# Kernel optimization log

Hardware: AMD Instinct MI355X
Metric: run time of the kernel (lower is better)

Reference implementation:

```python
import jax, jax.numpy as jnp
import numpy as np

TAU = 2.0   # LIF membrane time constant
VTH = 1.0   # spike threshold
EPS = 1e-5
T = 2       # spiking timesteps
H = 8       # attention heads
L = 4       # transformer depth
SCALE = 0.125
GW = 0.8    # graph branch weight


def _spike(v):
    # heaviside forward, sigmoid surrogate backward (spikingjelly-style)
    sg = jax.nn.sigmoid(4.0 * (v - VTH))
    return sg + jax.lax.stop_gradient((v >= VTH).astype(v.dtype) - sg)


def lif(x):
    # multi-step LIF over leading time axis, hard reset, detach_reset=True
    def step(v, xt):
        v = v + (xt - v) / TAU
        s = _spike(v)
        v = v * (1.0 - jax.lax.stop_gradient(s))
        return v, s
    _, s = jax.lax.scan(step, jnp.zeros_like(x[0]), x)
    return s


def bn(x, g, b):
    # batch-norm (training stats) over all dims but the channel dim
    ax = tuple(range(x.ndim - 1))
    m = x.mean(ax, keepdims=True)
    v = x.var(ax, keepdims=True)
    return (x - m) * jax.lax.rsqrt(v + EPS) * g + b


def ln(x, g, b):
    m = x.mean(-1, keepdims=True)
    v = x.var(-1, keepdims=True)
    return (x - m) * jax.lax.rsqrt(v + EPS) * g + b


def gcn_agg(x, row, col, n):
    # symmetric-normalized sparse aggregation: out[col] += x[row] / sqrt(d[row]d[col])
    deg = jax.ops.segment_sum(jnp.ones_like(col, dtype=x.dtype), col, num_segments=n)
    dinv = jnp.where(deg > 0, jax.lax.rsqrt(deg), 0.0)
    val = dinv[col] * dinv[row]
    return jax.ops.segment_sum(val[:, None] * x[row], col, num_segments=n)


def _forward(fl, edge_index):
    (x, fc0_w, fc0_b, ln_g, ln_b, wq, wk, wv, wo,
     bnq_g, bnq_b, bnk_g, bnk_b, bnv_g, bnv_b, bno_g, bno_b,
     w1, bn1_g, bn1_b, w2, bn2_g, bn2_b, head_w, head_b,
     gfc_w, gfc_b, gbn0_g, gbn0_b, gconv_w, gconv_b, gbn_g, gbn_b,
     fc_w, fc_b) = fl
    N = x.shape[0]
    row, col = edge_index[0], edge_index[1]
    # ---- spiking transformer branch: x -> [T,N,D] ----
    h = jnp.broadcast_to(x, (T,) + x.shape) @ fc0_w + fc0_b
    h = jax.nn.relu(ln(h, ln_g, ln_b))
    D = h.shape[-1]
    for l in range(L):
        s = lif(h)
        q = lif(bn(s @ wq[l], bnq_g[l], bnq_b[l])).reshape(T, N, H, D // H)
        k = lif(bn(s @ wk[l], bnk_g[l], bnk_b[l])).reshape(T, N, H, D // H)
        v = lif(bn(s @ wv[l], bnv_g[l], bnv_b[l])).reshape(T, N, H, D // H)
        # linear (token-sum) spiking self-attention: kv = K^T V per head/timestep
        kv = jnp.einsum('tnhd,tnhe->thde', k, v)
        o = (jnp.einsum('tnhd,thde->tnhe', q, kv) * SCALE).reshape(T, N, D)
        o = bn(lif(o) @ wo[l], bno_g[l], bno_b[l])
        h = h + o
        m = bn(lif(h) @ w1[l], bn1_g[l], bn1_b[l])
        m = bn(lif(m) @ w2[l], bn2_g[l], bn2_b[l])
        h = h + m
    x1 = (lif(h) @ head_w + head_b).mean(0)   # [N, C], mean over T (TET=False)
    # ---- sparse GNN diffusion branch ----
    g0 = jax.nn.relu(bn(x @ gfc_w + gfc_b, gbn0_g, gbn0_b))
    g = g0
    for i in range(2):
        g = gcn_agg(g, row, col, N) @ gconv_w[i] + gconv_b[i]
        g = jax.nn.relu(bn(g, gbn_g[i], gbn_b[i]))
        g = g + g0  # residual to first layer
    out = GW * g + (1.0 - GW) * x1
    return out @ fc_w + fc_b


def setup_inputs() -> dict:
    key = jax.random.key(0)
    ks = iter(jax.random.split(key, 64))
    N, F, D, C = 16384, 512, 512, 40
    DH = 2 * D
    r = lambda *s: jax.random.normal(next(ks), s, dtype=jnp.float32)
    inp = {
        'x': r(N, F),
        'fc0_w': r(F, D) * 0.02, 'fc0_b': jnp.zeros((D,), jnp.float32),
        'ln_g': jnp.ones((D,), jnp.float32), 'ln_b': jnp.zeros((D,), jnp.float32),
        'wq': r(L, D, D) * 0.02, 'wk': r(L, D, D) * 0.02,
        'wv': r(L, D, D) * 0.02, 'wo': r(L, D, D) * 0.02,
        'bnq_g': 1.0 + 0.1 * r(L, D), 'bnq_b': 0.02 * r(L, D),
        'bnk_g': 1.0 + 0.1 * r(L, D), 'bnk_b': 0.02 * r(L, D),
        'bnv_g': 1.0 + 0.1 * r(L, D), 'bnv_b': 0.02 * r(L, D),
        'bno_g': 1.0 + 0.1 * r(L, D), 'bno_b': 0.02 * r(L, D),
        'w1': r(L, D, DH) * 0.02, 'bn1_g': 1.0 + 0.1 * r(L, DH), 'bn1_b': 0.02 * r(L, DH),
        'w2': r(L, DH, D) * 0.02, 'bn2_g': 1.0 + 0.1 * r(L, D), 'bn2_b': 0.02 * r(L, D),
        'head_w': r(D, C) * 0.02, 'head_b': jnp.zeros((C,), jnp.float32),
        'gfc_w': r(F, C) * 0.02, 'gfc_b': jnp.zeros((C,), jnp.float32),
        'gbn0_g': jnp.ones((C,), jnp.float32), 'gbn0_b': jnp.zeros((C,), jnp.float32),
        'gconv_w': r(2, C, C) * 0.1, 'gconv_b': jnp.zeros((2, C), jnp.float32),
        'gbn_g': 1.0 + 0.1 * r(2, C), 'gbn_b': 0.02 * r(2, C),
        'fc_w': r(C, C) * 0.1, 'fc_b': jnp.zeros((C,), jnp.float32),
        'edge_index': jax.random.randint(next(ks), (2, 262144), 0, N, dtype=jnp.int32),
    }
    return inp


def reference(x, fc0_w, fc0_b, ln_g, ln_b, wq, wk, wv, wo, bnq_g, bnq_b, bnk_g, bnk_b, bnv_g, bnv_b, bno_g, bno_b, w1, bn1_g, bn1_b, w2, bn2_g, bn2_b, head_w, head_b, gfc_w, gfc_b, gbn0_g, gbn0_b, gconv_w, gconv_b, gbn_g, gbn_b, fc_w, fc_b, edge_index):
    fl = (x, fc0_w, fc0_b, ln_g, ln_b, wq, wk, wv, wo, bnq_g, bnq_b, bnk_g, bnk_b, bnv_g, bnv_b, bno_g, bno_b, w1, bn1_g, bn1_b, w2, bn2_g, bn2_b, head_w, head_b, gfc_w, gfc_b, gbn0_g, gbn0_b, gconv_w, gconv_b, gbn_g, gbn_b, fc_w, fc_b)
    return _forward(fl, edge_index)
```

## Files before the change

kernel.cpp:

```cpp
#include <hip/hip_runtime.h>
#include <cstddef>
#include <cstdint>

constexpr int N_NODES = 16384;
constexpr int D_MODEL = 512;
constexpr int C_OUT   = 40;
constexpr int CW      = 256;
constexpr int ND      = N_NODES * D_MODEL;
constexpr int M2      = 2 * N_NODES;

typedef int i32x4 __attribute__((ext_vector_type(4)));

#define S0 0.001953125
#define S1 1.52587890625e-05
#define S2 1.1920928955078125e-07
#define S3 9.31322574615478515625e-10
#define S4 7.2759576141834259033203125e-12

#define WD_Q 0
#define WD_K 1310720
#define WD_V 2621440
#define WD_O 3932160
#define WD_1 5242880
#define WD_2 7864320
#define WD_TOTAL 10485760

__global__ __launch_bounds__(256)
void w_digits_layer(const float* __restrict__ wq, const float* __restrict__ wk,
                    const float* __restrict__ wv, const float* __restrict__ wo,
                    const float* __restrict__ w1, const float* __restrict__ w2,
                    uint8_t* __restrict__ Wd) {
    int idx = blockIdx.x * 256 + threadIdx.x;
    const float* W;
    uint8_t* outb;
    int N, rem;
    if (idx < 1048576) {
        int mm = idx >> 18;
        rem = idx & 262143;
        const float* ptrs[4] = {wq, wk, wv, wo};
        W = ptrs[mm]; outb = Wd + (size_t)mm * 1310720; N = 512;
    } else if (idx < 1572864) {
        rem = idx - 1048576; W = w1; outb = Wd + WD_1; N = 1024;
    } else if (idx < 2097152) {
        rem = idx - 1572864; W = w2; outb = Wd + WD_2; N = 512;
    } else return;
    int k = rem / N, n = rem - k * N;
    double r = (double)W[rem];
    uint8_t* out = outb + (((size_t)(k >> 4) * N + n) * 5) * 16 + (k & 15);
    const double scl[5] = {512.0, 65536.0, 8388608.0, 1073741824.0, 137438953472.0};
    const double inv[5] = {S0, S1, S2, S3, S4};
#pragma unroll
    for (int j = 0; j < 5; ++j) {
        int d = (int)rint(r * scl[j]);
        d = d > 127 ? 127 : (d < -127 ? -127 : d);
        r -= (double)d * inv[j];
        out[j * 16] = (uint8_t)(int8_t)d;
    }
}

__global__ __launch_bounds__(256)
void gemm_i8_bits(const uint64_t* __restrict__ bits, int kWords,
                  const uint8_t* __restrict__ Wd, int Nmat, int colOff,
                  double* __restrict__ C, int ldc, int K,
                  double* __restrict__ sum, double* __restrict__ sumsq) {
    const int lane = threadIdx.x & 63;
    const int wv   = threadIdx.x >> 6;
    const int m    = lane & 15;
    const int q    = lane >> 4;
    const int row  = blockIdx.y * 64 + wv * 16 + m;
    const int colB = blockIdx.x * 64;

    i32x4 acc[4][5];
#pragma unroll
    for (int t = 0; t < 4; ++t)
#pragma unroll
        for (int j = 0; j < 5; ++j) acc[t][j] = (i32x4){0, 0, 0, 0};

    const uint64_t* brow = bits + (size_t)row * kWords;
    const size_t colBase = (size_t)(colOff + colB + m);

    for (int kb = 0; kb < K; kb += 64) {
        uint64_t wbits = brow[kb >> 6];
        uint32_t hw = (uint32_t)(wbits >> (q * 16)) & 0xFFFFu;
        i32x4 afrag;
#pragma unroll
        for (int i = 0; i < 4; ++i)
            afrag[i] = (int)((((hw >> (4 * i)) & 0xFu) * 0x00204081u) & 0x01010101u);

        const size_t kb4 = (size_t)(kb >> 4) + q;
        const uint8_t* bp = Wd + (kb4 * Nmat + colBase) * 80;
#pragma unroll
        for (int t = 0; t < 4; ++t) {
            const uint8_t* bt = bp + (size_t)t * 16 * 80;
#pragma unroll
            for (int j = 0; j < 5; ++j) {
                i32x4 bfrag = *reinterpret_cast<const i32x4*>(bt + j * 16);
                acc[t][j] = __builtin_amdgcn_mfma_i32_16x16x64_i8(afrag, bfrag, acc[t][j], 0, 0, 0);
            }
        }
    }

    const int orow = blockIdx.y * 64 + wv * 16 + q * 4;
    double sarr[4], qarr[4];
#pragma unroll
    for (int t = 0; t < 4; ++t) {
        double s = 0.0, qs = 0.0;
        double* Cc = C + (size_t)orow * ldc + colB + t * 16 + m;
#pragma unroll
        for (int i = 0; i < 4; ++i) {
            double p = (double)acc[t][0][i] * S0 + (double)acc[t][1][i] * S1
                     + (double)acc[t][2][i] * S2 + (double)acc[t][3][i] * S3
                     + (double)acc[t][4][i] * S4;
            Cc[(size_t)i * ldc] = p;
            s += p; qs += p * p;
        }
        sarr[t] = s; qarr[t] = qs;
    }
    __shared__ double ls[4][64], lq[4][64];
#pragma unroll
    for (int t = 0; t < 4; ++t) {
        double s = sarr[t], qq = qarr[t];
        s  += __shfl_xor(s, 16);  s  += __shfl_xor(s, 32);
        qq += __shfl_xor(qq, 16); qq += __shfl_xor(qq, 32);
        if (lane < 16) { ls[wv][t * 16 + lane] = s; lq[wv][t * 16 + lane] = qq; }
    }
    __syncthreads();
    if (threadIdx.x < 64) {
        int t = threadIdx.x;
        double s  = ls[0][t] + ls[1][t] + ls[2][t] + ls[3][t];
        double qq = lq[0][t] + lq[1][t] + lq[2][t] + lq[3][t];
        atomicAdd(&sum[colB + t], s);
        atomicAdd(&sumsq[colB + t], qq);
    }
}

__global__ __launch_bounds__(256)
void head_gather(const uint64_t* __restrict__ bits, const float* __restrict__ W,
                 const float* __restrict__ bias, float* __restrict__ Y) {
    const int lane = threadIdx.x & 63;
    const int wid  = threadIdx.x >> 6;
    const int r = blockIdx.x * 4 + wid;
    if (lane >= C_OUT) return;
    double acc = (double)bias[lane];
    const uint64_t* bw = bits + (size_t)r * 8;
    for (int j = 0; j < 8; ++j) {
        uint64_t w = bw[j];
        const float* Wk = W + (size_t)j * 64 * C_OUT + lane;
        while (w) {
            int k = __builtin_ctzll(w);
            w &= w - 1;
            acc += (double)Wk[(size_t)k * C_OUT];
        }
    }
    Y[(size_t)r * C_OUT + lane] = (float)acc;
}

__global__ __launch_bounds__(256)
void gemm_f32d(const float* __restrict__ A, int lda,
               const float* __restrict__ B, int ldb,
               const float* __restrict__ bias,
               double* __restrict__ C, int ldc, int M, int Nc, int K) {
    __shared__ double As[16][64];
    __shared__ double Bs[16][64];
    const int tid = threadIdx.x;
    const int tx  = tid & 15, ty = tid >> 4;
    const int row0 = blockIdx.y * 64 + ty * 4;
    const int col0 = blockIdx.x * 64 + tx * 4;
    const int ar = tid >> 2, ak = (tid & 3) * 4;
    const int bk = tid >> 4, bn = (tid & 15) * 4;
    const int gm = blockIdx.y * 64 + ar;
    double acc[4][4];
#pragma unroll
    for (int i = 0; i < 4; i++)
#pragma unroll
        for (int j = 0; j < 4; j++) acc[i][j] = 0.0;
    for (int k0 = 0; k0 < K; k0 += 16) {
#pragma unroll
        for (int j = 0; j < 4; j++)
            As[ak + j][ar] = (gm < M) ? (double)A[(size_t)gm * lda + k0 + ak + j] : 0.0;
#pragma unroll
        for (int j = 0; j < 4; j++) {
            int gn = blockIdx.x * 64 + bn + j;
            Bs[bk][bn + j] = (gn < Nc) ? (double)B[(size_t)(k0 + bk) * ldb + gn] : 0.0;
        }
        __syncthreads();
#pragma unroll
        for (int kk = 0; kk < 16; kk++) {
            double a4[4], b4[4];
#pragma unroll
            for (int i = 0; i < 4; i++) a4[i] = As[kk][ty * 4 + i];
#pragma unroll
            for (int j = 0; j < 4; j++) b4[j] = Bs[kk][tx * 4 + j];
#pragma unroll
            for (int i = 0; i < 4; i++)
#pragma unroll
                for (int j = 0; j < 4; j++) acc[i][j] = fma(a4[i], b4[j], acc[i][j]);
        }
        __syncthreads();
    }
#pragma unroll
    for (int i = 0; i < 4; i++) {
        int r = row0 + i;
        if (r >= M) continue;
#pragma unroll
        for (int j = 0; j < 4; j++) {
            int c = col0 + j;
            if (c < Nc) {
                double v = acc[i][j];
                if (bias) v += (double)bias[c];
                C[(size_t)r * ldc + c] = v;
            }
        }
    }
}

__global__ __launch_bounds__(256)
void gemm_f32(const float* __restrict__ A, int lda,
              const float* __restrict__ B, int ldb,
              const float* __restrict__ bias,
              float* __restrict__ C, int ldc, int M, int Nc, int K) {
    __shared__ float As[16][64];
    __shared__ float Bs[16][64];
    const int tid = threadIdx.x;
    const int tx  = tid & 15, ty = tid >> 4;
    const int row0 = blockIdx.y * 64 + ty * 4;
    const int col0 = blockIdx.x * 64 + tx * 4;
    const int ar = tid >> 2, ak = (tid & 3) * 4;
    const int bk = tid >> 4, bn = (tid & 15) * 4;
    const int gm = blockIdx.y * 64 + ar;
    double acc[4][4];
#pragma unroll
    for (int i = 0; i < 4; i++)
#pragma unroll
        for (int j = 0; j < 4; j++) acc[i][j] = 0.0;
    for (int k0 = 0; k0 < K; k0 += 16) {
#pragma unroll
        for (int j = 0; j < 4; j++) {
            int kk = k0 + ak + j;
            As[ak + j][ar] = (gm < M && kk < K) ? A[(size_t)gm * lda + kk] : 0.f;
        }
#pragma unroll
        for (int j = 0; j < 4; j++) {
            int gn = blockIdx.x * 64 + bn + j;
            int kk = k0 + bk;
            Bs[bk][bn + j] = (gn < Nc && kk < K) ? B[(size_t)kk * ldb + gn] : 0.f;
        }
        __syncthreads();
#pragma unroll
        for (int kk = 0; kk < 16; kk++) {
            float a4[4], b4[4];
#pragma unroll
            for (int i = 0; i < 4; i++) a4[i] = As[kk][ty * 4 + i];
#pragma unroll
            for (int j = 0; j < 4; j++) b4[j] = Bs[kk][tx * 4 + j];
#pragma unroll
            for (int i = 0; i < 4; i++)
#pragma unroll
                for (int j = 0; j < 4; j++) acc[i][j] = fma((double)a4[i], (double)b4[j], acc[i][j]);
        }
        __syncthreads();
    }
#pragma unroll
    for (int i = 0; i < 4; i++) {
        int r = row0 + i;
        if (r >= M) continue;
#pragma unroll
        for (int j = 0; j < 4; j++) {
            int c = col0 + j;
            if (c < Nc) {
                double v = acc[i][j];
                if (bias) v += (double)bias[c];
                C[(size_t)r * ldc + c] = (float)v;
            }
        }
    }
}

__global__ __launch_bounds__(256)
void col_stats_f(const float* __restrict__ X, int M, int Ch, int rowsPerBlock,
                 double* __restrict__ sum, double* __restrict__ sumsq) {
    const int cl = threadIdx.x & 63;
    const int c  = blockIdx.x * 64 + cl;
    const int rg = threadIdx.x >> 6;
    const int r0 = blockIdx.y * rowsPerBlock;
    const int r1 = min(r0 + rowsPerBlock, M);
    double s = 0.0, q = 0.0;
    if (c < Ch) {
        for (int r = r0 + rg; r < r1; r += 4) {
            double v = (double)X[(size_t)r * Ch + c];
            s += v; q += v * v;
        }
    }
    __shared__ double ls[4][64], lq[4][64];
    ls[rg][cl] = s; lq[rg][cl] = q;
    __syncthreads();
    if (rg == 0 && c < Ch) {
        s = ls[0][cl] + ls[1][cl] + ls[2][cl] + ls[3][cl];
        q = lq[0][cl] + lq[1][cl] + lq[2][cl] + lq[3][cl];
        atomicAdd(&sum[c], s);
        atomicAdd(&sumsq[c], q);
    }
}

__device__ __forceinline__ void lif2(double x0, double x1, bool& s0, bool& s1) {
    double v = x0 * 0.5;
    s0 = (v >= 1.0);
    v = s0 ? 0.0 : v;
    v = v + (x1 - v) * 0.5;
    s1 = (v >= 1.0);
}

__device__ __forceinline__ void bn_params(const double* sum, const double* sumsq,
                                          const float* g, const float* b, double invM,
                                          int c, double& sc, double& sh) {
    double m   = sum[c] * invM;
    double var = sumsq[c] * invM - m * m;
    sc = (double)g[c] / sqrt(var + 1e-5);
    sh = (double)b[c] - m * sc;
}

__global__ __launch_bounds__(256)
void lif_bits_f(const float* __restrict__ O, uint64_t* __restrict__ S) {
    int i = blockIdx.x * 256 + threadIdx.x;
    bool s0, s1;
    lif2((double)O[i], (double)O[(size_t)i + ND], s0, s1);
    uint64_t b0 = __ballot(s0), b1 = __ballot(s1);
    if ((threadIdx.x & 63) == 0) {
        int widx = i >> 6;
        S[widx] = b0;
        S[widx + N_NODES * 8] = b1;
    }
}

__global__ __launch_bounds__(256)
void bn_lif_bits2(const double* __restrict__ X,
                  const double* __restrict__ sum, const double* __restrict__ sumsq,
                  const float* __restrict__ g, const float* __restrict__ b, double invM,
                  uint64_t* __restrict__ S, int osWords, int chOffWords) {
    int i = blockIdx.x * 256 + threadIdx.x;
    int n = i >> 8, c = i & 255;
    double sc, sh;
    bn_params(sum, sumsq, g, b, invM, c, sc, sh);
    bool s0, s1;
    lif2((double)X[i] * sc + sh, (double)X[(size_t)i + (size_t)N_NODES * 256] * sc + sh, s0, s1);
    uint64_t b0 = __ballot(s0), b1 = __ballot(s1);
    if ((threadIdx.x & 63) == 0) {
        int widx = n * osWords + chOffWords + (c >> 6);
        S[widx] = b0;
        S[widx + N_NODES * osWords] = b1;
    }
}

__global__ __launch_bounds__(256)
void bn_add_lif2(const double* __restrict__ X,
                 const double* __restrict__ sum, const double* __restrict__ sumsq,
                 const float* __restrict__ g, const float* __restrict__ b, double invM,
                 double* __restrict__ H, int chOff, uint64_t* __restrict__ S) {
    int i = blockIdx.x * 256 + threadIdx.x;
    int n = i >> 8, c = i & 255;
    double sc, sh;
    bn_params(sum, sumsq, g, b, invM, c, sc, sh);
    size_t hi = (size_t)n * 512 + chOff + c;
    double h0 = H[hi] + ((double)X[i] * sc + sh);
    double h1 = H[hi + ND] + ((double)X[(size_t)i + (size_t)N_NODES * 256] * sc + sh);
    H[hi] = h0;
    H[hi + ND] = h1;
    bool s0, s1;
    lif2(h0, h1, s0, s1);
    uint64_t b0 = __ballot(s0), b1 = __ballot(s1);
    if ((threadIdx.x & 63) == 0) {
        int widx = n * 8 + (chOff >> 6) + (c >> 6);
        S[widx] = b0;
        S[widx + N_NODES * 8] = b1;
    }
}

__global__ __launch_bounds__(256)
void ln_relu_lif(const double* __restrict__ X, const float* __restrict__ g,
                 const float* __restrict__ b, double* __restrict__ H,
                 uint64_t* __restrict__ S) {
    int n = blockIdx.x;
    const double* x = X + (size_t)n * 512;
    int c0 = threadIdx.x, c1 = threadIdx.x + 256;
    double v0 = x[c0], v1 = x[c1];
    __shared__ double ls[256], lq[256];
    ls[threadIdx.x] = v0 + v1;
    lq[threadIdx.x] = v0 * v0 + v1 * v1;
    __syncthreads();
    for (int off = 128; off > 0; off >>= 1) {
        if (threadIdx.x < off) {
            ls[threadIdx.x] += ls[threadIdx.x + off];
            lq[threadIdx.x] += lq[threadIdx.x + off];
        }
        __syncthreads();
    }
    double m    = ls[0] * (1.0 / 512);
    double var  = lq[0] * (1.0 / 512) - m * m;
    double rstd = 1.0 / sqrt(var + 1e-5);
    double o0 = (v0 - m) * rstd * (double)g[c0] + (double)b[c0];
    double o1 = (v1 - m) * rstd * (double)g[c1] + (double)b[c1];
    o0 = o0 > 0.0 ? o0 : 0.0;
    o1 = o1 > 0.0 ? o1 : 0.0;
    double* h0 = H + (size_t)n * 512;
    h0[c0] = o0; h0[c1] = o1;
    h0[ND + c0] = o0; h0[ND + c1] = o1;
    bool a0, a1, d0, d1;
    lif2(o0, o0, a0, a1);
    lif2(o1, o1, d0, d1);
    uint64_t ba0 = __ballot(a0), ba1 = __ballot(a1);
    uint64_t bd0 = __ballot(d0), bd1 = __ballot(d1);
    if ((threadIdx.x & 63) == 0) {
        int w = threadIdx.x >> 6;
        S[n * 8 + w] = ba0;
        S[n * 8 + w + N_NODES * 8] = ba1;
        S[n * 8 + 4 + w] = bd0;
        S[n * 8 + 4 + w + N_NODES * 8] = bd1;
    }
}

__global__ __launch_bounds__(256)
void kv_bits(const uint64_t* __restrict__ Kb, const uint64_t* __restrict__ Vb,
             float* __restrict__ KV, int nPerBlock) {
    const int th = blockIdx.x;
    const int t = th >> 3, h = th & 7;
    const int nbase = blockIdx.y * nPerBlock;
    const int e = threadIdx.x & 63, dg = threadIdx.x >> 6;
    float acc[16];
#pragma unroll
    for (int i = 0; i < 16; i++) acc[i] = 0.f;
    __shared__ float ks[8][64], vs[8][64];
    const size_t wbase = (size_t)t * N_NODES * 8 + h;
    for (int n0 = 0; n0 < nPerBlock; n0 += 8) {
        for (int idx = threadIdx.x; idx < 8 * 128; idx += 256) {
            int r = idx >> 7, c = idx & 127;
            size_t wi = wbase + (size_t)(nbase + n0 + r) * 8;
            if (c < 64) ks[r][c] = (float)((Kb[wi] >> c) & 1ull);
            else        vs[r][c - 64] = (float)((Vb[wi] >> (c - 64)) & 1ull);
        }
        __syncthreads();
#pragma unroll
        for (int r = 0; r < 8; ++r) {
            float ve = vs[r][e];
#pragma unroll
            for (int i = 0; i < 16; ++i) acc[i] += ks[r][dg * 16 + i] * ve;
        }
        __syncthreads();
    }
    float* kvp = KV + (size_t)th * 4096;
    for (int i = 0; i < 16; ++i)
        atomicAdd(&kvp[(dg * 16 + i) * 64 + e], acc[i]);
}

__global__ __launch_bounds__(256)
void o_bits(const uint64_t* __restrict__ Qb, const float* __restrict__ KV,
            float* __restrict__ O) {
    const int th = blockIdx.y;
    const int t = th >> 3, h = th & 7;
    const int nb = blockIdx.x;
    __shared__ float kvs[64][64];
    __shared__ float qs[64][65];
    const float* kvp = KV + (size_t)th * 4096;
    for (int idx = threadIdx.x; idx < 4096; idx += 256)
        kvs[idx >> 6][idx & 63] = kvp[idx];
    const size_t wbase = ((size_t)t * N_NODES + (size_t)nb * 64) * 8 + h;
    for (int idx = threadIdx.x; idx < 4096; idx += 256) {
        int r = idx >> 6, c = idx & 63;
        qs[r][c] = (float)((Qb[wbase + (size_t)r * 8] >> c) & 1ull);
    }
    __syncthreads();
    const int e = threadIdx.x & 63, rg = threadIdx.x >> 6;
    float acc[16];
#pragma unroll
    for (int i = 0; i < 16; i++) acc[i] = 0.f;
    for (int d = 0; d < 64; ++d) {
        float kv = kvs[d][e];
#pragma unroll
        for (int i = 0; i < 16; ++i) acc[i] += qs[rg * 16 + i][d] * kv;
    }
    const size_t obase = ((size_t)t * N_NODES + (size_t)nb * 64) * 512 + (size_t)h * 64;
    for (int i = 0; i < 16; ++i)
        O[obase + (size_t)(rg * 16 + i) * 512 + e] = acc[i] * 0.125f;
}

__global__ __launch_bounds__(256)
void deg_kernel(const int* __restrict__ col, float* __restrict__ deg, int E) {
    int e = blockIdx.x * 256 + threadIdx.x;
    if (e < E) atomicAdd(&deg[col[e]], 1.0f);
}

__global__ __launch_bounds__(256)
void dinv_kernel(float* __restrict__ deg, int n) {
    int i = blockIdx.x * 256 + threadIdx.x;
    if (i < n) {
        double d = (double)deg[i];
        deg[i] = d > 0.0 ? (float)(1.0 / sqrt(d)) : 0.f;
    }
}

__global__ __launch_bounds__(256)
void agg_kernel(const float* __restrict__ G, const int* __restrict__ row,
                const int* __restrict__ col, const float* __restrict__ dinv,
                float* __restrict__ out, int E) {
    int idx = blockIdx.x * 256 + threadIdx.x;
    int e = idx >> 6, c = idx & 63;
    if (e >= E || c >= C_OUT) return;
    int r = row[e], cl = col[e];
    float val = dinv[cl] * dinv[r];
    atomicAdd(&out[(size_t)cl * C_OUT + c], val * G[(size_t)r * C_OUT + c]);
}

__global__ __launch_bounds__(256)
void bn_relu_add_f2(const float* __restrict__ X,
                    const double* __restrict__ sum, const double* __restrict__ sumsq,
                    const float* __restrict__ g, const float* __restrict__ b, double invM,
                    const float* __restrict__ add, float* __restrict__ out, int NC, int Ch) {
    int i = blockIdx.x * 256 + threadIdx.x;
    if (i >= NC) return;
    int c = i % Ch;
    double sc, sh;
    bn_params(sum, sumsq, g, b, invM, c, sc, sh);
    double v = (double)X[i] * sc + sh;
    v = v > 0.0 ? v : 0.0;
    if (add) v += (double)add[i];
    out[i] = (float)v;
}

__global__ __launch_bounds__(256)
void mix_kernel(const float* __restrict__ G, const float* __restrict__ Y,
                float* __restrict__ P, int NC) {
    int i = blockIdx.x * 256 + threadIdx.x;
    if (i >= NC) return;
    double y = 0.5 * ((double)Y[i] + (double)Y[(size_t)i + NC]);
    P[i] = (float)(0.8 * (double)G[i] + 0.2 * y);
}

__global__ __launch_bounds__(256)
void final_fc_kernel(const float* __restrict__ A, const float* __restrict__ W,
                     const float* __restrict__ bias, float* __restrict__ out) {
    __shared__ float Ws[40][40];
    for (int idx = threadIdx.x; idx < 1600; idx += 256)
        Ws[idx / 40][idx % 40] = W[idx];
    __syncthreads();
    int i = blockIdx.x * 256 + threadIdx.x;
    if (i >= N_NODES * C_OUT) return;
    int n = i / 40, c = i - n * 40;
    const float* a = A + (size_t)n * 40;
    double acc = (double)bias[c];
#pragma unroll 8
    for (int k = 0; k < 40; ++k) acc += (double)a[k] * (double)Ws[k][c];
    out[i] = (float)acc;
}

static inline dim3 grid1(long n) { return dim3((unsigned)((n + 255) / 256)); }

extern "C" void kernel_launch(void* const* d_in, const int* in_sizes, int n_in,
                              void* d_out, int out_size, void* d_ws, size_t ws_size,
                              hipStream_t stream) {
    const float* x      = (const float*)d_in[0];
    const float* fc0_w  = (const float*)d_in[1];
    const float* fc0_b  = (const float*)d_in[2];
    const float* ln_g   = (const float*)d_in[3];
    const float* ln_b   = (const float*)d_in[4];
    const float* wq     = (const float*)d_in[5];
    const float* wk     = (const float*)d_in[6];
    const float* wv     = (const float*)d_in[7];
    const float* wo     = (const float*)d_in[8];
    const float* bnq_g  = (const float*)d_in[9];
    const float* bnq_b  = (const float*)d_in[10];
    const float* bnk_g  = (const float*)d_in[11];
    const float* bnk_b  = (const float*)d_in[12];
    const float* bnv_g  = (const float*)d_in[13];
    const float* bnv_b  = (const float*)d_in[14];
    const float* bno_g  = (const float*)d_in[15];
    const float* bno_b  = (const float*)d_in[16];
    const float* w1     = (const float*)d_in[17];
    const float* bn1_g  = (const float*)d_in[18];
    const float* bn1_b  = (const float*)d_in[19];
    const float* w2     = (const float*)d_in[20];
    const float* bn2_g  = (const float*)d_in[21];
    const float* bn2_b  = (const float*)d_in[22];
    const float* head_w = (const float*)d_in[23];
    const float* head_b = (const float*)d_in[24];
    const float* gfc_w  = (const float*)d_in[25];
    const float* gfc_b  = (const float*)d_in[26];
    const float* gbn0_g = (const float*)d_in[27];
    const float* gbn0_b = (const float*)d_in[28];
    const float* gconv_w= (const float*)d_in[29];
    const float* gconv_b= (const float*)d_in[30];
    const float* gbn_g  = (const float*)d_in[31];
    const float* gbn_b  = (const float*)d_in[32];
    const float* fc_w   = (const float*)d_in[33];
    const float* fc_b   = (const float*)d_in[34];
    const int*   edge   = (const int*)d_in[35];

    const int E = in_sizes[35] / 2;
    const int* erow = edge;
    const int* ecol = edge + E;
    const int NC = N_NODES * C_OUT;

    uint8_t* wsbase = (uint8_t*)d_ws;
    size_t off = 0;
    auto alloc = [&](size_t bytes, size_t align) -> void* {
        off = (off + align - 1) & ~(align - 1);
        void* p = wsbase + off;
        off += bytes;
        return p;
    };
    double*   statBuf = (double*)alloc((size_t)64 * 512 * sizeof(double), 256);
    double*   h_buf  = (double*)alloc((size_t)2 * ND * sizeof(double), 256);
    double*   Pd     = (double*)alloc((size_t)M2 * CW * sizeof(double), 256);
    float*    O32    = (float*)Pd;
    uint8_t*  Wdig   = (uint8_t*)alloc((size_t)WD_TOTAL, 256);
    uint64_t* s_bits = (uint64_t*)alloc((size_t)2 * N_NODES * 8 * 8, 256);
    uint64_t* q_bits = (uint64_t*)alloc((size_t)2 * N_NODES * 8 * 8, 256);
    uint64_t* k_bits = (uint64_t*)alloc((size_t)2 * N_NODES * 8 * 8, 256);
    uint64_t* v_bits = (uint64_t*)alloc((size_t)2 * N_NODES * 8 * 8, 256);
    uint64_t* m_bits = (uint64_t*)alloc((size_t)2 * N_NODES * 16 * 8, 256);
    float*    ybuf   = (float*)m_bits;
    (void)alloc((size_t)2 * NC * sizeof(float) > (size_t)2 * N_NODES * 16 * 8
                ? (size_t)2 * NC * sizeof(float) - (size_t)2 * N_NODES * 16 * 8 : 0, 256);
    float*    g0     = (float*)alloc((size_t)NC * sizeof(float), 256);
    float*    gg     = (float*)alloc((size_t)NC * sizeof(float), 256);
    float*    ag     = (float*)alloc((size_t)NC * sizeof(float), 256);
    float*    kvb    = (float*)alloc((size_t)65536 * sizeof(float), 256);
    float*    deg    = (float*)alloc((size_t)N_NODES * sizeof(float), 256);
    if (off > ws_size) return;

    const dim3 blk(256);
    const dim3 gLIF((unsigned)(ND / 256));
    const dim3 gCHK((unsigned)(N_NODES));
    const dim3 gGEMM(CW / 64, M2 / 64);
    const double invM2 = 1.0 / (double)M2;
    const double invMN = 1.0 / (double)N_NODES;

    hipMemsetAsync(statBuf, 0, (size_t)64 * 512 * sizeof(double), stream);

    int gate = 0;
    auto nextStat = [&]() { return statBuf + (size_t)(gate++) * 512; };

    hipLaunchKernelGGL(gemm_f32d, dim3(8, N_NODES / 64), blk, 0, stream,
                       x, 512, fc0_w, 512, fc0_b, Pd, 512, N_NODES, 512, 512);
    hipLaunchKernelGGL(ln_relu_lif, dim3(N_NODES), blk, 0, stream, Pd, ln_g, ln_b, h_buf, s_bits);

    for (int l = 0; l < 4; ++l) {
        hipLaunchKernelGGL(w_digits_layer, dim3(8192), blk, 0, stream,
                           wq + (size_t)l * 262144, wk + (size_t)l * 262144,
                           wv + (size_t)l * 262144, wo + (size_t)l * 262144,
                           w1 + (size_t)l * 524288, w2 + (size_t)l * 524288, Wdig);

        uint64_t* qkvb[3] = {q_bits, k_bits, v_bits};
        const size_t wdoff[3] = {WD_Q, WD_K, WD_V};
        const float* gmat[3] = {bnq_g + l * 512, bnk_g + l * 512, bnv_g + l * 512};
        const float* bmat[3] = {bnq_b + l * 512, bnk_b + l * 512, bnv_b + l * 512};
        for (int j = 0; j < 3; ++j) {
            for (int c0 = 0; c0 < 512; c0 += CW) {
                double* st = nextStat();
                hipLaunchKernelGGL(gemm_i8_bits, gGEMM, blk, 0, stream,
                                   s_bits, 8, Wdig + wdoff[j], 512, c0, Pd, CW, 512, st, st + 256);
                hipLaunchKernelGGL(bn_lif_bits2, gCHK, blk, 0, stream,
                                   Pd, st, st + 256, gmat[j] + c0, bmat[j] + c0, invM2,
                                   qkvb[j], 8, c0 / 64);
            }
        }

        hipMemsetAsync(kvb, 0, 65536 * sizeof(float), stream);
        hipLaunchKernelGGL(kv_bits, dim3(16, 16), blk, 0, stream, k_bits, v_bits, kvb, 1024);
        hipLaunchKernelGGL(o_bits, dim3(N_NODES / 64, 16), blk, 0, stream, q_bits, kvb, O32);
        hipLaunchKernelGGL(lif_bits_f, gLIF, blk, 0, stream, O32, q_bits);

        for (int c0 = 0; c0 < 512; c0 += CW) {
            double* st = nextStat();
            hipLaunchKernelGGL(gemm_i8_bits, gGEMM, blk, 0, stream,
                               q_bits, 8, Wdig + WD_O, 512, c0, Pd, CW, 512, st, st + 256);
            hipLaunchKernelGGL(bn_add_lif2, gCHK, blk, 0, stream,
                               Pd, st, st + 256, bno_g + l * 512 + c0, bno_b + l * 512 + c0,
                               invM2, h_buf, c0, s_bits);
        }

        for (int c0 = 0; c0 < 1024; c0 += CW) {
            double* st = nextStat();
            hipLaunchKernelGGL(gemm_i8_bits, gGEMM, blk, 0, stream,
                               s_bits, 8, Wdig + WD_1, 1024, c0, Pd, CW, 512, st, st + 256);
            hipLaunchKernelGGL(bn_lif_bits2, gCHK, blk, 0, stream,
                               Pd, st, st + 256, bn1_g + l * 1024 + c0, bn1_b + l * 1024 + c0,
                               invM2, m_bits, 16, c0 / 64);
        }
        for (int c0 = 0; c0 < 512; c0 += CW) {
            double* st = nextStat();
            hipLaunchKernelGGL(gemm_i8_bits, gGEMM, blk, 0, stream,
                               m_bits, 16, Wdig + WD_2, 512, c0, Pd, CW, 1024, st, st + 256);
            hipLaunchKernelGGL(bn_add_lif2, gCHK, blk, 0, stream,
                               Pd, st, st + 256, bn2_g + l * 512 + c0, bn2_b + l * 512 + c0,
                               invM2, h_buf, c0, s_bits);
        }
    }

    hipLaunchKernelGGL(head_gather, dim3(M2 / 4), blk, 0, stream, s_bits, head_w, head_b, ybuf);

    hipLaunchKernelGGL(gemm_f32, dim3(1, N_NODES / 64), blk, 0, stream,
                       x, 512, gfc_w, 40, gfc_b, ag, 40, N_NODES, 40, 512);
    {
        double* st = nextStat();
        dim3 gs(1, (N_NODES + 511) / 512);
        hipLaunchKernelGGL(col_stats_f, gs, blk, 0, stream, ag, N_NODES, 40, 512, st, st + 256);
        hipLaunchKernelGGL(bn_relu_add_f2, grid1(NC), blk, 0, stream,
                           ag, st, st + 256, gbn0_g, gbn0_b, invMN,
                           (const float*)nullptr, g0, NC, 40);
    }

    hipMemsetAsync(deg, 0, N_NODES * sizeof(float), stream);
    hipLaunchKernelGGL(deg_kernel, grid1(E), blk, 0, stream, ecol, deg, E);
    hipLaunchKernelGGL(dinv_kernel, grid1(N_NODES), blk, 0, stream, deg, N_NODES);

    const float* gsrc = g0;
    for (int i = 0; i < 2; ++i) {
        hipMemsetAsync(ag, 0, (size_t)NC * sizeof(float), stream);
        hipLaunchKernelGGL(agg_kernel, grid1((long)E * 64), blk, 0, stream,
                           gsrc, erow, ecol, deg, ag, E);
        hipLaunchKernelGGL(gemm_f32, dim3(1, N_NODES / 64), blk, 0, stream,
                           ag, 40, gconv_w + (size_t)i * 40 * 40, 40, gconv_b + i * 40,
                           gg, 40, N_NODES, 40, 40);
        double* st = nextStat();
        dim3 gs(1, (N_NODES + 511) / 512);
        hipLaunchKernelGGL(col_stats_f, gs, blk, 0, stream, gg, N_NODES, 40, 512, st, st + 256);
        hipLaunchKernelGGL(bn_relu_add_f2, grid1(NC), blk, 0, stream,
                           gg, st, st + 256, gbn_g + i * 40, gbn_b + i * 40, invMN, g0, gg, NC, 40);
        gsrc = gg;
    }

    hipLaunchKernelGGL(mix_kernel, grid1(NC), blk, 0, stream, gg, ybuf, ag, NC);
    hipLaunchKernelGGL(final_fc_kernel, grid1((long)N_NODES * C_OUT), blk, 0, stream,
                       ag, fc_w, fc_b, (float*)d_out);
}
```

Measured before the change: 6.958 ms.

## Stage weight digits in LDS and double row tile per wave in int8 GEMM

```diff
diff --git a/kernel.cpp b/kernel.cpp
--- a/kernel.cpp
+++ b/kernel.cpp
@@ -34,28 +34,36 @@
     const float* W;
     uint8_t* outb;
     int N, rem;
-    if (idx < 1048576) {
-        int mm = idx >> 18;
-        rem = idx & 262143;
+    if (idx < 65536) {
+        int mm = idx >> 14;
+        rem = idx & 16383;
         const float* ptrs[4] = {wq, wk, wv, wo};
         W = ptrs[mm]; outb = Wd + (size_t)mm * 1310720; N = 512;
-    } else if (idx < 1572864) {
-        rem = idx - 1048576; W = w1; outb = Wd + WD_1; N = 1024;
-    } else if (idx < 2097152) {
-        rem = idx - 1572864; W = w2; outb = Wd + WD_2; N = 512;
-    } else return;
-    int k = rem / N, n = rem - k * N;
-    double r = (double)W[rem];
-    uint8_t* out = outb + (((size_t)(k >> 4) * N + n) * 5) * 16 + (k & 15);
+    } else if (idx < 98304) {
+        rem = idx - 65536; W = w1; outb = Wd + WD_1; N = 1024;
+    } else {
+        rem = idx - 98304; W = w2; outb = Wd + WD_2; N = 512;
+    }
+    int kg = rem / N, n = rem - kg * N;
+    const float* Wp = W + (size_t)kg * 16 * N + n;
+    uint8_t* out = outb + (size_t)(kg * N + n) * 80;
     const double scl[5] = {512.0, 65536.0, 8388608.0, 1073741824.0, 137438953472.0};
     const double inv[5] = {S0, S1, S2, S3, S4};
-#pragma unroll
-    for (int j = 0; j < 5; ++j) {
-        int d = (int)rint(r * scl[j]);
-        d = d > 127 ? 127 : (d < -127 ? -127 : d);
-        r -= (double)d * inv[j];
-        out[j * 16] = (uint8_t)(int8_t)d;
-    }
+    union { uint8_t b[5][16]; i32x4 v[5]; } db;
+#pragma unroll
+    for (int kk = 0; kk < 16; ++kk) {
+        double r = (double)Wp[(size_t)kk * N];
+#pragma unroll
+        for (int j = 0; j < 5; ++j) {
+            int d = (int)rint(r * scl[j]);
+            d = d > 127 ? 127 : (d < -127 ? -127 : d);
+            r -= (double)d * inv[j];
+            db.b[j][kk] = (uint8_t)(int8_t)d;
+        }
+    }
+#pragma unroll
+    for (int j = 0; j < 5; ++j)
+        *reinterpret_cast<i32x4*>(out + j * 16) = db.v[j];
 }
 
 __global__ __launch_bounds__(256)
@@ -63,58 +71,89 @@
                   const uint8_t* __restrict__ Wd, int Nmat, int colOff,
                   double* __restrict__ C, int ldc, int K,
                   double* __restrict__ sum, double* __restrict__ sumsq) {
+    __shared__ __attribute__((aligned(16))) uint8_t Bs[20480];
     const int lane = threadIdx.x & 63;
     const int wv   = threadIdx.x >> 6;
     const int m    = lane & 15;
     const int q    = lane >> 4;
-    const int row  = blockIdx.y * 64 + wv * 16 + m;
+    const int rowT = blockIdx.y * 128 + wv * 32;
     const int colB = blockIdx.x * 64;
 
-    i32x4 acc[4][5];
-#pragma unroll
-    for (int t = 0; t < 4; ++t)
-#pragma unroll
-        for (int j = 0; j < 5; ++j) acc[t][j] = (i32x4){0, 0, 0, 0};
-
-    const uint64_t* brow = bits + (size_t)row * kWords;
-    const size_t colBase = (size_t)(colOff + colB + m);
+    i32x4 acc[2][4][5];
+#pragma unroll
+    for (int rt = 0; rt < 2; ++rt)
+#pragma unroll
+        for (int t = 0; t < 4; ++t)
+#pragma unroll
+            for (int j = 0; j < 5; ++j) acc[rt][t][j] = (i32x4){0, 0, 0, 0};
+
+    const uint64_t* brow0 = bits + (size_t)(rowT + m) * kWords;
+    const uint64_t* brow1 = brow0 + (size_t)16 * kWords;
+    const size_t cb = (size_t)(colOff + colB);
 
     for (int kb = 0; kb < K; kb += 64) {
-        uint64_t wbits = brow[kb >> 6];
-        uint32_t hw = (uint32_t)(wbits >> (q * 16)) & 0xFFFFu;
-        i32x4 afrag;
-#pragma unroll
-        for (int i = 0; i < 4; ++i)
-            afrag[i] = (int)((((hw >> (4 * i)) & 0xFu) * 0x00204081u) & 0x01010101u);
-
-        const size_t kb4 = (size_t)(kb >> 4) + q;
-        const uint8_t* bp = Wd + (kb4 * Nmat + colBase) * 80;
+        i32x4 tmp[5];
+        const size_t kt0 = (size_t)(kb >> 4);
+#pragma unroll
+        for (int c5 = 0; c5 < 5; ++c5) {
+            int c  = threadIdx.x + c5 * 256;
+            int kt = c / 320;
+            int of = c - kt * 320;
+            tmp[c5] = *reinterpret_cast<const i32x4*>(
+                Wd + ((kt0 + (size_t)kt) * Nmat + cb) * 80 + (size_t)of * 16);
+        }
+        uint64_t wb0 = brow0[kb >> 6];
+        uint64_t wb1 = brow1[kb >> 6];
+        uint32_t hw0 = (uint32_t)(wb0 >> (q * 16)) & 0xFFFFu;
+        uint32_t hw1 = (uint32_t)(wb1 >> (q * 16)) & 0xFFFFu;
+        i32x4 af0, af1;
+#pragma unroll
+        for (int i = 0; i < 4; ++i) {
+            af0[i] = (int)((((hw0 >> (4 * i)) & 0xFu) * 0x00204081u) & 0x01010101u);
+            af1[i] = (int)((((hw1 >> (4 * i)) & 0xFu) * 0x00204081u) & 0x01010101u);
+        }
+        __syncthreads();
+#pragma unroll
+        for (int c5 = 0; c5 < 5; ++c5) {
+            int c  = threadIdx.x + c5 * 256;
+            int kt = c / 320;
+            int of = c - kt * 320;
+            *reinterpret_cast<i32x4*>(Bs + kt * 5120 + of * 16) = tmp[c5];
+        }
+        __syncthreads();
 #pragma unroll
         for (int t = 0; t < 4; ++t) {
-            const uint8_t* bt = bp + (size_t)t * 16 * 80;
+            const uint8_t* bt = Bs + q * 5120 + (t * 16 + m) * 80;
+            i32x4 bf[5];
+#pragma unroll
+            for (int j = 0; j < 5; ++j)
+                bf[j] = *reinterpret_cast<const i32x4*>(bt + j * 16);
 #pragma unroll
             for (int j = 0; j < 5; ++j) {
-                i32x4 bfrag = *reinterpret_cast<const i32x4*>(bt + j * 16);
-                acc[t][j] = __builtin_amdgcn_mfma_i32_16x16x64_i8(afrag, bfrag, acc[t][j], 0, 0, 0);
+                acc[0][t][j] = __builtin_amdgcn_mfma_i32_16x16x64_i8(af0, bf[j], acc[0][t][j], 0, 0, 0);
+                acc[1][t][j] = __builtin_amdgcn_mfma_i32_16x16x64_i8(af1, bf[j], acc[1][t][j], 0, 0, 0);
             }
         }
     }
 
-    const int orow = blockIdx.y * 64 + wv * 16 + q * 4;
     double sarr[4], qarr[4];
 #pragma unroll
-    for (int t = 0; t < 4; ++t) {
-        double s = 0.0, qs = 0.0;
-        double* Cc = C + (size_t)orow * ldc + colB + t * 16 + m;
-#pragma unroll
-        for (int i = 0; i < 4; ++i) {
-            double p = (double)acc[t][0][i] * S0 + (double)acc[t][1][i] * S1
-                     + (double)acc[t][2][i] * S2 + (double)acc[t][3][i] * S3
-                     + (double)acc[t][4][i] * S4;
-            Cc[(size_t)i * ldc] = p;
-            s += p; qs += p * p;
-        }
-        sarr[t] = s; qarr[t] = qs;
+    for (int t = 0; t < 4; ++t) { sarr[t] = 0.0; qarr[t] = 0.0; }
+#pragma unroll
+    for (int rt = 0; rt < 2; ++rt) {
+        const int orow = rowT + rt * 16 + q * 4;
+#pragma unroll
+        for (int t = 0; t < 4; ++t) {
+            double* Cc = C + (size_t)orow * ldc + colB + t * 16 + m;
+#pragma unroll
+            for (int i = 0; i < 4; ++i) {
+                double p = (double)acc[rt][t][0][i] * S0 + (double)acc[rt][t][1][i] * S1
+                         + (double)acc[rt][t][2][i] * S2 + (double)acc[rt][t][3][i] * S3
+                         + (double)acc[rt][t][4][i] * S4;
+                Cc[(size_t)i * ldc] = p;
+                sarr[t] += p; qarr[t] += p * p;
+            }
+        }
     }
     __shared__ double ls[4][64], lq[4][64];
 #pragma unroll
@@ -629,7 +668,7 @@
     const dim3 blk(256);
     const dim3 gLIF((unsigned)(ND / 256));
     const dim3 gCHK((unsigned)(N_NODES));
-    const dim3 gGEMM(CW / 64, M2 / 64);
+    const dim3 gGEMM(CW / 64, M2 / 128);
     const double invM2 = 1.0 / (double)M2;
     const double invMN = 1.0 / (double)N_NODES;
 
@@ -643,7 +682,7 @@
     hipLaunchKernelGGL(ln_relu_lif, dim3(N_NODES), blk, 0, stream, Pd, ln_g, ln_b, h_buf, s_bits);
 
     for (int l = 0; l < 4; ++l) {
-        hipLaunchKernelGGL(w_digits_layer, dim3(8192), blk, 0, stream,
+        hipLaunchKernelGGL(w_digits_layer, dim3(512), blk, 0, stream,
                            wq + (size_t)l * 262144, wk + (size_t)l * 262144,
                            wv + (size_t)l * 262144, wo + (size_t)l * 262144,
                            w1 + (size_t)l * 524288, w2 + (size_t)l * 524288, Wdig);
```

Result: faster. 6.726 ms (-3.3%).
